# Kernel optimization log

Hardware: AMD Instinct MI355X
Metric: run time of the kernel (lower is better)

## Reference

```python
import jax, jax.numpy as jnp
import numpy as np

BINS = 50
MIN_V = 0.0
MAX_V = 1.0
SIGMA = 10.0
DELTA = (MAX_V - MIN_V) / BINS
EPS = 1e-8


def _soft_bin(v, centers):
    # v: [N, D] -> [N, bins, D]
    d = v[:, None, :] - centers[None, :, None]
    return jax.nn.sigmoid(SIGMA * (d + DELTA / 2)) - jax.nn.sigmoid(SIGMA * (d - DELTA / 2))


def setup_inputs() -> dict:
    key = jax.random.key(0)
    k1, k2 = jax.random.split(key)
    im1 = jax.random.uniform(k1, (8, 384, 384), dtype=jnp.float32)
    im2 = jax.random.uniform(k2, (8, 384, 384), dtype=jnp.float32)
    return {"im1": im1, "im2": im2}


def reference(im1, im2):
    n = im1.shape[0]
    x = im1.reshape(n, -1)
    y = im2.reshape(n, -1)
    centers = MIN_V + DELTA * (jnp.arange(BINS, dtype=jnp.float32) + 0.5)
    xs = _soft_bin(x, centers)  # [N, bins, D]
    ys = _soft_bin(y, centers)  # [N, bins, D]
    hgram = jnp.einsum('nbd,ncd->nbc', xs, ys)  # [N, bins, bins]
    # NOTE: original normalizes by the sum over the WHOLE batch
    p_xy = hgram / jnp.sum(hgram)
    marginal_x = jnp.sum(p_xy, axis=2)  # [N, bins]
    marginal_y = jnp.sum(p_xy, axis=1)  # [N, bins]
    joined = marginal_x[:, :, None] * marginal_y[:, None, :]  # [N, bins, bins]
    mi_per = jnp.sum(
        p_xy * (jnp.log(p_xy + EPS) - jnp.log(joined + EPS)), axis=(1, 2)
    )
    return jnp.sum(mi_per)  # reduction='sum'
```

## Files before the change

### kernel.cpp

```cpp
#include <hip/hip_runtime.h>


#define D_TOTAL   147456
#define NBATCH    8
#define BINS      50
#define NEDGE     28
#define KSLICES   192
#define KC        128
#define SLICE_LEN (D_TOTAL / KSLICES)
#define ITERS     (SLICE_LEN / KC)
#define LDS_STR   152

typedef _Float16 half8 __attribute__((ext_vector_type(8)));
typedef float    f32x4 __attribute__((ext_vector_type(4)));

__global__ __launch_bounds__(256, 6) void hgram_kernel(const float* __restrict__ im1,
                                                       const float* __restrict__ im2,
                                                       float* __restrict__ hg) {
    __shared__ __align__(16) _Float16 Xs[32][LDS_STR];
    __shared__ __align__(16) _Float16 Ys[32][LDS_STR];

    const int tid   = threadIdx.x;
    const int slice = blockIdx.x;
    const int n     = blockIdx.y;
    const int base  = n * D_TOTAL + slice * SLICE_LEN;

    {
        unsigned* px = (unsigned*)&Xs[0][0];
        unsigned* py = (unsigned*)&Ys[0][0];
        for (int i = tid; i < 32 * LDS_STR / 2; i += 256) { px[i] = 0u; py[i] = 0u; }
    }
    __syncthreads();

    const int col = tid & 127;
    const int isY = tid >> 7;
    const float*  src = isY ? im2 : im1;
    _Float16*     dst = isY ? &Ys[0][0] : &Xs[0][0];

    const int lane = tid & 63;
    const int w    = tid >> 6;
    const int r0   = (w & 1) << 4;
    const int c0   = (w >> 1) << 4;
    const int frow = lane & 15;
    const int kg   = (lane >> 4) << 3;

    f32x4 acc = {0.f, 0.f, 0.f, 0.f};

    for (int it = 0; it < ITERS; ++it) {
        {
            float v = src[base + it * KC + col];
            float E = __builtin_amdgcn_exp2f(v * -14.426950408889634f);
            float u = E * 0.6703200460356393f;
            #pragma unroll
            for (int i = 0; i < NEDGE; ++i) {
                float t = __builtin_amdgcn_rcpf(__builtin_fmaf(u, 0.00390625f, 0.00390625f));
                dst[i * LDS_STR + col] = (_Float16)t;
                u *= 1.4918246976412703f;
            }
        }
        __syncthreads();
        #pragma unroll
        for (int ks = 0; ks < 4; ++ks) {
            const int k0 = ks * 32 + kg;
            half8 a = *(const half8*)&Xs[r0 + frow][k0];
            half8 b = *(const half8*)&Ys[c0 + frow][k0];
            acc = __builtin_amdgcn_mfma_f32_16x16x32_f16(a, b, acc, 0, 0, 0);
        }
        __syncthreads();
    }

    float* hgn = hg + n * 1024;
    const int gj = c0 + (lane & 15);
    const int ri = r0 + ((lane >> 4) << 2);
    if (gj < NEDGE) {
        #pragma unroll
        for (int r = 0; r < 4; ++r) {
            const int gi = ri + r;
            if (gi < NEDGE) atomicAdd(&hgn[gi * 32 + gj], acc[r]);
        }
    }
}

__global__ __launch_bounds__(1024) void finalize_kernel(const float* __restrict__ hg,
                                                        float* __restrict__ out) {
    __shared__ float Gs[NBATCH][NEDGE][29];
    __shared__ float mx[NBATCH][BINS], my[NBATCH][BINS];
    __shared__ float red[16];
    __shared__ float sT;
    const int tid = threadIdx.x;

    for (int idx = tid; idx < NBATCH * NEDGE * NEDGE; idx += 1024) {
        int n = idx / (NEDGE * NEDGE);
        int rem = idx - n * NEDGE * NEDGE;
        int r = rem / NEDGE, c = rem - r * NEDGE;
        Gs[n][r][c] = hg[n * 1024 + r * 32 + c];
    }
    __syncthreads();

    if (tid < 2 * NBATCH * BINS) {
        const int which = (tid >= NBATCH * BINS) ? 1 : 0;
        const int t2 = which ? tid - NBATCH * BINS : tid;
        const int n = t2 / BINS, b = t2 - n * BINS;
        const int q = b >> 1;
        float w0, w1, w2, w3;
        if (b & 1) { w0 = -1.f; w1 = 9.f; w2 = -7.f; w3 = -1.f; }
        else       { w0 =  1.f; w1 = 7.f; w2 = -9.f; w3 =  1.f; }
        float m;
        if (which == 0) {
            m = w0 * (Gs[n][q][1]   - Gs[n][q][26])
              + w1 * (Gs[n][q+1][1] - Gs[n][q+1][26])
              + w2 * (Gs[n][q+2][1] - Gs[n][q+2][26])
              + w3 * (Gs[n][q+3][1] - Gs[n][q+3][26]);
            mx[n][b] = m * 0.0625f;
        } else {
            m = w0 * (Gs[n][1][q]   - Gs[n][26][q])
              + w1 * (Gs[n][1][q+1] - Gs[n][26][q+1])
              + w2 * (Gs[n][1][q+2] - Gs[n][26][q+2])
              + w3 * (Gs[n][1][q+3] - Gs[n][26][q+3]);
            my[n][b] = m * 0.0625f;
        }
    }
    if (tid == 0) {
        float t = 0.f;
        for (int n = 0; n < NBATCH; ++n)
            t += Gs[n][1][1] - Gs[n][1][26] - Gs[n][26][1] + Gs[n][26][26];
        sT = t;
    }
    __syncthreads();

    const float invT = 1.0f / sT;
    const float invT2 = invT * invT;
    float mi = 0.f;
    for (int task = tid; task < NBATCH * 25 * 25; task += 1024) {
        const int n = task / 625;
        const int rem = task - n * 625;
        const int bp = rem / 25, cp = rem - bp * 25;
        float g[4][4];
        #pragma unroll
        for (int r = 0; r < 4; ++r)
            #pragma unroll
            for (int s = 0; s < 4; ++s) g[r][s] = Gs[n][bp + r][cp + s];
        float rde[4], rdo[4];
        #pragma unroll
        for (int r = 0; r < 4; ++r) {
            rde[r] =  g[r][0] + 7.f * g[r][1] - 9.f * g[r][2] + g[r][3];
            rdo[r] = -g[r][0] + 9.f * g[r][1] - 7.f * g[r][2] - g[r][3];
        }
        const float hee = ( rde[0] + 7.f*rde[1] - 9.f*rde[2] + rde[3]) * (1.f/256.f);
        const float heo = ( rdo[0] + 7.f*rdo[1] - 9.f*rdo[2] + rdo[3]) * (1.f/256.f);
        const float hoe = (-rde[0] + 9.f*rde[1] - 7.f*rde[2] - rde[3]) * (1.f/256.f);
        const float hoo = (-rdo[0] + 9.f*rdo[1] - 7.f*rdo[2] - rdo[3]) * (1.f/256.f);
        const int b0 = 2 * bp, c0 = 2 * cp;
        {
            float p = hee * invT, jo = mx[n][b0] * my[n][c0] * invT2;
            mi += p * (__logf(p + 1e-8f) - __logf(jo + 1e-8f));
        }
        {
            float p = heo * invT, jo = mx[n][b0] * my[n][c0 + 1] * invT2;
            mi += p * (__logf(p + 1e-8f) - __logf(jo + 1e-8f));
        }
        {
            float p = hoe * invT, jo = mx[n][b0 + 1] * my[n][c0] * invT2;
            mi += p * (__logf(p + 1e-8f) - __logf(jo + 1e-8f));
        }
        {
            float p = hoo * invT, jo = mx[n][b0 + 1] * my[n][c0 + 1] * invT2;
            mi += p * (__logf(p + 1e-8f) - __logf(jo + 1e-8f));
        }
    }
    #pragma unroll
    for (int o = 32; o > 0; o >>= 1) mi += __shfl_down(mi, o, 64);
    if ((tid & 63) == 0) red[tid >> 6] = mi;
    __syncthreads();
    if (tid == 0) {
        float t = 0.f;
        for (int i = 0; i < 16; ++i) t += red[i];
        out[0] = t;
    }
}

extern "C" void kernel_launch(void* const* d_in, const int* in_sizes, int n_in,
                              void* d_out, int out_size, void* d_ws, size_t ws_size,
                              hipStream_t stream) {
    const float* im1 = (const float*)d_in[0];
    const float* im2 = (const float*)d_in[1];
    float* out = (float*)d_out;
    float* hg  = (float*)d_ws;

    hipMemsetAsync(d_ws, 0, NBATCH * 1024 * sizeof(float), stream);
    hgram_kernel<<<dim3(KSLICES, NBATCH), dim3(256), 0, stream>>>(im1, im2, hg);
    finalize_kernel<<<dim3(1), dim3(1024), 0, stream>>>(hg, out);
}
```

Measured before the change: 89.17 us.

## Fuse finalize into histogram kernel via last-block reduction and double-buffer LDS

Merges the finalize kernel into the histogram kernel. The last block to finish, detected with an atomic counter, reads the accumulated histogram and computes the MI sum, which removes one kernel launch. The LDS staging is double-buffered so the next tile's global load and sigmoid-edge staging overlap the MFMA step, dropping one barrier per iteration. Slice count drops from 192 to 128 per batch and launch bounds are lowered. The tail now runs on a single 256-thread block instead of 1024 threads.

```diff
diff --git a/kernel.cpp b/kernel.cpp
--- a/kernel.cpp
+++ b/kernel.cpp
@@ -5,37 +5,41 @@
 #define NBATCH    8
 #define BINS      50
 #define NEDGE     28
-#define KSLICES   192
+#define KSLICES   128
 #define KC        128
 #define SLICE_LEN (D_TOTAL / KSLICES)
 #define ITERS     (SLICE_LEN / KC)
 #define LDS_STR   152
+#define NBLOCKS   (KSLICES * NBATCH)
 
 typedef _Float16 half8 __attribute__((ext_vector_type(8)));
 typedef float    f32x4 __attribute__((ext_vector_type(4)));
 
-__global__ __launch_bounds__(256, 6) void hgram_kernel(const float* __restrict__ im1,
-                                                       const float* __restrict__ im2,
-                                                       float* __restrict__ hg) {
-    __shared__ __align__(16) _Float16 Xs[32][LDS_STR];
-    __shared__ __align__(16) _Float16 Ys[32][LDS_STR];
+__global__ __launch_bounds__(256, 4) void mi_kernel(const float* __restrict__ im1,
+                                                    const float* __restrict__ im2,
+                                                    float* __restrict__ hg,
+                                                    unsigned* __restrict__ done,
+                                                    float* __restrict__ out) {
+    __shared__ __align__(16) _Float16 S[2][2][32][LDS_STR];
+    __shared__ unsigned last_flag;
+    __shared__ float red[4];
+    __shared__ float sTv;
 
     const int tid   = threadIdx.x;
     const int slice = blockIdx.x;
     const int n     = blockIdx.y;
     const int base  = n * D_TOTAL + slice * SLICE_LEN;
 
-    {
-        unsigned* px = (unsigned*)&Xs[0][0];
-        unsigned* py = (unsigned*)&Ys[0][0];
-        for (int i = tid; i < 32 * LDS_STR / 2; i += 256) { px[i] = 0u; py[i] = 0u; }
-    }
-    __syncthreads();
+    for (int i = tid; i < 4 * 304; i += 256) {
+        const int p = i >> 8 << 8 ? 0 : 0;
+        const int plane = i / 304;
+        const int q = i - plane * 304;
+        ((unsigned*)&S[plane >> 1][plane & 1][28][0])[q] = 0u;
+    }
 
     const int col = tid & 127;
     const int isY = tid >> 7;
-    const float*  src = isY ? im2 : im1;
-    _Float16*     dst = isY ? &Ys[0][0] : &Xs[0][0];
+    const float* src = isY ? im2 : im1;
 
     const int lane = tid & 63;
     const int w    = tid >> 6;
@@ -46,100 +50,111 @@
 
     f32x4 acc = {0.f, 0.f, 0.f, 0.f};
 
+    auto stage = [&](int buf, float v) {
+        _Float16* dst = &S[buf][isY][0][col];
+        float E = __builtin_amdgcn_exp2f(v * -14.426950408889634f);
+        float u = E * 0.6703200460356393f;
+        #pragma unroll
+        for (int i = 0; i < NEDGE; ++i) {
+            float t = __builtin_amdgcn_rcpf(__builtin_fmaf(u, 0.00390625f, 0.00390625f));
+            dst[i * LDS_STR] = (_Float16)t;
+            u *= 1.4918246976412703f;
+        }
+    };
+
+    stage(0, src[base + col]);
     for (int it = 0; it < ITERS; ++it) {
-        {
-            float v = src[base + it * KC + col];
-            float E = __builtin_amdgcn_exp2f(v * -14.426950408889634f);
-            float u = E * 0.6703200460356393f;
-            #pragma unroll
-            for (int i = 0; i < NEDGE; ++i) {
-                float t = __builtin_amdgcn_rcpf(__builtin_fmaf(u, 0.00390625f, 0.00390625f));
-                dst[i * LDS_STR + col] = (_Float16)t;
-                u *= 1.4918246976412703f;
-            }
-        }
+        float vn = 0.f;
+        if (it + 1 < ITERS) vn = src[base + (it + 1) * KC + col];
         __syncthreads();
+        const int buf = it & 1;
         #pragma unroll
         for (int ks = 0; ks < 4; ++ks) {
             const int k0 = ks * 32 + kg;
-            half8 a = *(const half8*)&Xs[r0 + frow][k0];
-            half8 b = *(const half8*)&Ys[c0 + frow][k0];
+            half8 a = *(const half8*)&S[buf][0][r0 + frow][k0];
+            half8 b = *(const half8*)&S[buf][1][c0 + frow][k0];
             acc = __builtin_amdgcn_mfma_f32_16x16x32_f16(a, b, acc, 0, 0, 0);
         }
-        __syncthreads();
-    }
-
-    float* hgn = hg + n * 1024;
-    const int gj = c0 + (lane & 15);
-    const int ri = r0 + ((lane >> 4) << 2);
-    if (gj < NEDGE) {
-        #pragma unroll
-        for (int r = 0; r < 4; ++r) {
-            const int gi = ri + r;
-            if (gi < NEDGE) atomicAdd(&hgn[gi * 32 + gj], acc[r]);
-        }
-    }
-}
-
-__global__ __launch_bounds__(1024) void finalize_kernel(const float* __restrict__ hg,
-                                                        float* __restrict__ out) {
-    __shared__ float Gs[NBATCH][NEDGE][29];
-    __shared__ float mx[NBATCH][BINS], my[NBATCH][BINS];
-    __shared__ float red[16];
-    __shared__ float sT;
-    const int tid = threadIdx.x;
-
-    for (int idx = tid; idx < NBATCH * NEDGE * NEDGE; idx += 1024) {
-        int n = idx / (NEDGE * NEDGE);
-        int rem = idx - n * NEDGE * NEDGE;
-        int r = rem / NEDGE, c = rem - r * NEDGE;
-        Gs[n][r][c] = hg[n * 1024 + r * 32 + c];
-    }
-    __syncthreads();
-
-    if (tid < 2 * NBATCH * BINS) {
-        const int which = (tid >= NBATCH * BINS) ? 1 : 0;
-        const int t2 = which ? tid - NBATCH * BINS : tid;
-        const int n = t2 / BINS, b = t2 - n * BINS;
+        if (it + 1 < ITERS) stage(buf ^ 1, vn);
+    }
+
+    {
+        float* hgn = hg + n * 1024;
+        const int gj = c0 + (lane & 15);
+        const int ri = r0 + ((lane >> 4) << 2);
+        if (gj < NEDGE) {
+            #pragma unroll
+            for (int r = 0; r < 4; ++r) {
+                const int gi = ri + r;
+                if (gi < NEDGE) atomicAdd(&hgn[gi * 32 + gj], acc[r]);
+            }
+        }
+    }
+    __threadfence();
+    __syncthreads();
+    if (tid == 0) last_flag = (atomicAdd(done, 1u) == NBLOCKS - 1) ? 1u : 0u;
+    __syncthreads();
+    if (!last_flag) return;
+
+    float* Gs = (float*)&S[0][0][0][0];
+    float* mx = Gs + NBATCH * 28 * 29;
+    float* my = mx + NBATCH * BINS;
+
+    for (int idx = tid; idx < NBATCH * 784; idx += 256) {
+        const int nn = idx / 784;
+        const int rem = idx - nn * 784;
+        const int r = rem / 28, c = rem - r * 28;
+        Gs[(nn * 28 + r) * 29 + c] = atomicAdd(&hg[nn * 1024 + r * 32 + c], 0.0f);
+    }
+    __syncthreads();
+
+    for (int t = tid; t < 2 * NBATCH * BINS; t += 256) {
+        const int which = (t >= NBATCH * BINS) ? 1 : 0;
+        const int t2 = which ? t - NBATCH * BINS : t;
+        const int nn = t2 / BINS, b = t2 - nn * BINS;
         const int q = b >> 1;
         float w0, w1, w2, w3;
         if (b & 1) { w0 = -1.f; w1 = 9.f; w2 = -7.f; w3 = -1.f; }
         else       { w0 =  1.f; w1 = 7.f; w2 = -9.f; w3 =  1.f; }
+        const float* G = &Gs[nn * 28 * 29];
         float m;
         if (which == 0) {
-            m = w0 * (Gs[n][q][1]   - Gs[n][q][26])
-              + w1 * (Gs[n][q+1][1] - Gs[n][q+1][26])
-              + w2 * (Gs[n][q+2][1] - Gs[n][q+2][26])
-              + w3 * (Gs[n][q+3][1] - Gs[n][q+3][26]);
-            mx[n][b] = m * 0.0625f;
+            m = w0 * (G[q * 29 + 1]       - G[q * 29 + 26])
+              + w1 * (G[(q + 1) * 29 + 1] - G[(q + 1) * 29 + 26])
+              + w2 * (G[(q + 2) * 29 + 1] - G[(q + 2) * 29 + 26])
+              + w3 * (G[(q + 3) * 29 + 1] - G[(q + 3) * 29 + 26]);
+            mx[nn * BINS + b] = m * 0.0625f;
         } else {
-            m = w0 * (Gs[n][1][q]   - Gs[n][26][q])
-              + w1 * (Gs[n][1][q+1] - Gs[n][26][q+1])
-              + w2 * (Gs[n][1][q+2] - Gs[n][26][q+2])
-              + w3 * (Gs[n][1][q+3] - Gs[n][26][q+3]);
-            my[n][b] = m * 0.0625f;
+            m = w0 * (G[1 * 29 + q]       - G[26 * 29 + q])
+              + w1 * (G[1 * 29 + q + 1]   - G[26 * 29 + q + 1])
+              + w2 * (G[1 * 29 + q + 2]   - G[26 * 29 + q + 2])
+              + w3 * (G[1 * 29 + q + 3]   - G[26 * 29 + q + 3]);
+            my[nn * BINS + b] = m * 0.0625f;
         }
     }
     if (tid == 0) {
         float t = 0.f;
-        for (int n = 0; n < NBATCH; ++n)
-            t += Gs[n][1][1] - Gs[n][1][26] - Gs[n][26][1] + Gs[n][26][26];
-        sT = t;
-    }
-    __syncthreads();
-
-    const float invT = 1.0f / sT;
+        for (int nn = 0; nn < NBATCH; ++nn) {
+            const float* G = &Gs[nn * 28 * 29];
+            t += G[1 * 29 + 1] - G[1 * 29 + 26] - G[26 * 29 + 1] + G[26 * 29 + 26];
+        }
+        sTv = t;
+    }
+    __syncthreads();
+
+    const float invT = 1.0f / sTv;
     const float invT2 = invT * invT;
     float mi = 0.f;
-    for (int task = tid; task < NBATCH * 25 * 25; task += 1024) {
-        const int n = task / 625;
-        const int rem = task - n * 625;
+    for (int task = tid; task < NBATCH * 625; task += 256) {
+        const int nn = task / 625;
+        const int rem = task - nn * 625;
         const int bp = rem / 25, cp = rem - bp * 25;
+        const float* G = &Gs[nn * 28 * 29];
         float g[4][4];
         #pragma unroll
         for (int r = 0; r < 4; ++r)
             #pragma unroll
-            for (int s = 0; s < 4; ++s) g[r][s] = Gs[n][bp + r][cp + s];
+            for (int s = 0; s < 4; ++s) g[r][s] = G[(bp + r) * 29 + (cp + s)];
         float rde[4], rdo[4];
         #pragma unroll
         for (int r = 0; r < 4; ++r) {
@@ -150,21 +165,21 @@
         const float heo = ( rdo[0] + 7.f*rdo[1] - 9.f*rdo[2] + rdo[3]) * (1.f/256.f);
         const float hoe = (-rde[0] + 9.f*rde[1] - 7.f*rde[2] - rde[3]) * (1.f/256.f);
         const float hoo = (-rdo[0] + 9.f*rdo[1] - 7.f*rdo[2] - rdo[3]) * (1.f/256.f);
-        const int b0 = 2 * bp, c0 = 2 * cp;
-        {
-            float p = hee * invT, jo = mx[n][b0] * my[n][c0] * invT2;
-            mi += p * (__logf(p + 1e-8f) - __logf(jo + 1e-8f));
-        }
-        {
-            float p = heo * invT, jo = mx[n][b0] * my[n][c0 + 1] * invT2;
-            mi += p * (__logf(p + 1e-8f) - __logf(jo + 1e-8f));
-        }
-        {
-            float p = hoe * invT, jo = mx[n][b0 + 1] * my[n][c0] * invT2;
-            mi += p * (__logf(p + 1e-8f) - __logf(jo + 1e-8f));
-        }
-        {
-            float p = hoo * invT, jo = mx[n][b0 + 1] * my[n][c0 + 1] * invT2;
+        const int b0 = 2 * bp, c0i = 2 * cp;
+        {
+            float p = hee * invT, jo = mx[nn * BINS + b0] * my[nn * BINS + c0i] * invT2;
+            mi += p * (__logf(p + 1e-8f) - __logf(jo + 1e-8f));
+        }
+        {
+            float p = heo * invT, jo = mx[nn * BINS + b0] * my[nn * BINS + c0i + 1] * invT2;
+            mi += p * (__logf(p + 1e-8f) - __logf(jo + 1e-8f));
+        }
+        {
+            float p = hoe * invT, jo = mx[nn * BINS + b0 + 1] * my[nn * BINS + c0i] * invT2;
+            mi += p * (__logf(p + 1e-8f) - __logf(jo + 1e-8f));
+        }
+        {
+            float p = hoo * invT, jo = mx[nn * BINS + b0 + 1] * my[nn * BINS + c0i + 1] * invT2;
             mi += p * (__logf(p + 1e-8f) - __logf(jo + 1e-8f));
         }
     }
@@ -172,11 +187,7 @@
     for (int o = 32; o > 0; o >>= 1) mi += __shfl_down(mi, o, 64);
     if ((tid & 63) == 0) red[tid >> 6] = mi;
     __syncthreads();
-    if (tid == 0) {
-        float t = 0.f;
-        for (int i = 0; i < 16; ++i) t += red[i];
-        out[0] = t;
-    }
+    if (tid == 0) out[0] = red[0] + red[1] + red[2] + red[3];
 }
 
 extern "C" void kernel_launch(void* const* d_in, const int* in_sizes, int n_in,
@@ -186,8 +197,8 @@
     const float* im2 = (const float*)d_in[1];
     float* out = (float*)d_out;
     float* hg  = (float*)d_ws;
-
-    hipMemsetAsync(d_ws, 0, NBATCH * 1024 * sizeof(float), stream);
-    hgram_kernel<<<dim3(KSLICES, NBATCH), dim3(256), 0, stream>>>(im1, im2, hg);
-    finalize_kernel<<<dim3(1), dim3(1024), 0, stream>>>(hg, out);
+    unsigned* done = (unsigned*)((char*)d_ws + NBATCH * 1024 * sizeof(float));
+
+    hipMemsetAsync(d_ws, 0, NBATCH * 1024 * sizeof(float) + sizeof(unsigned), stream);
+    mi_kernel<<<dim3(KSLICES, NBATCH), dim3(256), 0, stream>>>(im1, im2, hg, done, out);
 }
```

Measured after the change: 155.1 us. 1.74x slower.

## Widen K chunk, prefetch next inputs, split sigmoid chains for ILP

Applied to the files above, without the earlier changes.

Doubles the per-iteration K chunk to 256 columns, so each thread now produces soft-bin edge values for both images at its column. The sigmoid recurrence is split into four independent chains to give the scheduler more independent work. The next chunk's input values are loaded into registers before the current chunk is computed, hiding global latency. Only the four padding rows of the LDS tiles are zeroed, and one upfront barrier is dropped. Fewer barriers per element and more latency hiding are traded for larger LDS use and lower occupancy, with launch bounds reduced to 4.

```diff
diff --git a/kernel.cpp b/kernel.cpp
--- a/kernel.cpp
+++ b/kernel.cpp
@@ -6,15 +6,15 @@
 #define BINS      50
 #define NEDGE     28
 #define KSLICES   192
-#define KC        128
+#define KC        256
 #define SLICE_LEN (D_TOTAL / KSLICES)
 #define ITERS     (SLICE_LEN / KC)
-#define LDS_STR   152
+#define LDS_STR   280
 
 typedef _Float16 half8 __attribute__((ext_vector_type(8)));
 typedef float    f32x4 __attribute__((ext_vector_type(4)));
 
-__global__ __launch_bounds__(256, 6) void hgram_kernel(const float* __restrict__ im1,
+__global__ __launch_bounds__(256, 4) void hgram_kernel(const float* __restrict__ im1,
                                                        const float* __restrict__ im2,
                                                        float* __restrict__ hg) {
     __shared__ __align__(16) _Float16 Xs[32][LDS_STR];
@@ -26,17 +26,12 @@
     const int base  = n * D_TOTAL + slice * SLICE_LEN;
 
     {
-        unsigned* px = (unsigned*)&Xs[0][0];
-        unsigned* py = (unsigned*)&Ys[0][0];
-        for (int i = tid; i < 32 * LDS_STR / 2; i += 256) { px[i] = 0u; py[i] = 0u; }
-    }
-    __syncthreads();
-
-    const int col = tid & 127;
-    const int isY = tid >> 7;
-    const float*  src = isY ? im2 : im1;
-    _Float16*     dst = isY ? &Ys[0][0] : &Xs[0][0];
-
+        unsigned* px = (unsigned*)&Xs[28][0];
+        unsigned* py = (unsigned*)&Ys[28][0];
+        for (int i = tid; i < 4 * LDS_STR / 2; i += 256) { px[i] = 0u; py[i] = 0u; }
+    }
+
+    const int col  = tid;
     const int lane = tid & 63;
     const int w    = tid >> 6;
     const int r0   = (w & 1) << 4;
@@ -44,29 +39,51 @@
     const int frow = lane & 15;
     const int kg   = (lane >> 4) << 3;
 
+    auto stage1 = [&](float v, _Float16* dst) {
+        const float E = __builtin_amdgcn_exp2f(v * -14.426950408889634f);
+        float u0 = E * 0.6703200460356393f;
+        float u1 = E * 11.023176380641601f;
+        float u2 = E * 181.27224187515122f;
+        float u3 = E * 2980.9579870417283f;
+        #pragma unroll
+        for (int k = 0; k < 7; ++k) {
+            float t0 = __builtin_amdgcn_rcpf(__builtin_fmaf(u0, 0.00390625f, 0.00390625f));
+            float t1 = __builtin_amdgcn_rcpf(__builtin_fmaf(u1, 0.00390625f, 0.00390625f));
+            float t2 = __builtin_amdgcn_rcpf(__builtin_fmaf(u2, 0.00390625f, 0.00390625f));
+            float t3 = __builtin_amdgcn_rcpf(__builtin_fmaf(u3, 0.00390625f, 0.00390625f));
+            dst[(k)      * LDS_STR] = (_Float16)t0;
+            dst[(7 + k)  * LDS_STR] = (_Float16)t1;
+            dst[(14 + k) * LDS_STR] = (_Float16)t2;
+            dst[(21 + k) * LDS_STR] = (_Float16)t3;
+            u0 *= 1.4918246976412703f;
+            u1 *= 1.4918246976412703f;
+            u2 *= 1.4918246976412703f;
+            u3 *= 1.4918246976412703f;
+        }
+    };
+
     f32x4 acc = {0.f, 0.f, 0.f, 0.f};
 
+    float vx = im1[base + col];
+    float vy = im2[base + col];
     for (int it = 0; it < ITERS; ++it) {
-        {
-            float v = src[base + it * KC + col];
-            float E = __builtin_amdgcn_exp2f(v * -14.426950408889634f);
-            float u = E * 0.6703200460356393f;
-            #pragma unroll
-            for (int i = 0; i < NEDGE; ++i) {
-                float t = __builtin_amdgcn_rcpf(__builtin_fmaf(u, 0.00390625f, 0.00390625f));
-                dst[i * LDS_STR + col] = (_Float16)t;
-                u *= 1.4918246976412703f;
-            }
-        }
+        float nvx = 0.f, nvy = 0.f;
+        if (it + 1 < ITERS) {
+            nvx = im1[base + (it + 1) * KC + col];
+            nvy = im2[base + (it + 1) * KC + col];
+        }
+        stage1(vx, &Xs[0][col]);
+        stage1(vy, &Ys[0][col]);
         __syncthreads();
         #pragma unroll
-        for (int ks = 0; ks < 4; ++ks) {
+        for (int ks = 0; ks < 8; ++ks) {
             const int k0 = ks * 32 + kg;
             half8 a = *(const half8*)&Xs[r0 + frow][k0];
             half8 b = *(const half8*)&Ys[c0 + frow][k0];
             acc = __builtin_amdgcn_mfma_f32_16x16x32_f16(a, b, acc, 0, 0, 0);
         }
         __syncthreads();
+        vx = nvx; vy = nvy;
     }
 
     float* hgn = hg + n * 1024;
@@ -91,7 +108,7 @@
 
     for (int idx = tid; idx < NBATCH * NEDGE * NEDGE; idx += 1024) {
         int n = idx / (NEDGE * NEDGE);
-        int rem = idx - n * NEDGE * NEDGE;
+        int rem = idx - n * (NEDGE * NEDGE);
         int r = rem / NEDGE, c = rem - r * NEDGE;
         Gs[n][r][c] = hg[n * 1024 + r * 32 + c];
     }
```

Result: no change. 87.84 us (-1.5%).
